# Optimization experiments

Measured on AMD Instinct MI355X. Metric: run time of the kernel, lower is better.

The kernel has to match this reference:

```python
import jax, jax.numpy as jnp
import numpy as np

B, T, C = 2, 2048, 1024
H = 16
HD = C // H  # head_dim = 64
SCALE = HD ** -0.5

def setup_inputs() -> dict:
    key = jax.random.key(0)
    ks = jax.random.split(key, 5)
    s = 1.0 / np.sqrt(C)
    return {
        "x": jax.random.normal(ks[0], (B, T, C), dtype=jnp.float32),
        "Wq": jax.random.normal(ks[1], (C, C), dtype=jnp.float32) * s,
        "Wk": jax.random.normal(ks[2], (C, C), dtype=jnp.float32) * s,
        "Wv": jax.random.normal(ks[3], (C, C), dtype=jnp.float32) * s,
        "Wp": jax.random.normal(ks[4], (C, C), dtype=jnp.float32) * s,
        "bp": jnp.zeros((C,), dtype=jnp.float32),
    }

def reference(x, Wq, Wk, Wv, Wp, bp):
    b, t, c = x.shape
    # QKV projections (no bias, qkv_bias=False) -> [B,T,H,HD]
    q = (x @ Wq).reshape(b, t, H, HD)
    k = (x @ Wk).reshape(b, t, H, HD)
    v = (x @ Wv).reshape(b, t, H, HD)
    # scores [B,H,T,T]
    scores = jnp.einsum("bqhd,bkhd->bhqk", q, k) * SCALE
    causal = jnp.tril(jnp.ones((t, t), dtype=bool))
    scores = jnp.where(causal, scores, -jnp.inf)
    attn = jax.nn.softmax(scores, axis=-1)  # dropout = identity (eval mode)
    out = jnp.einsum("bhqk,bkhd->bqhd", attn, v).reshape(b, t, c)
    return out @ Wp + bp
```

## Files before the change

### kernel.cpp

```cpp
#include <hip/hip_runtime.h>


typedef __attribute__((ext_vector_type(8))) short shortx8;
typedef __attribute__((ext_vector_type(4))) short shortx4;
typedef __attribute__((ext_vector_type(8))) unsigned short ushortx8;
typedef __attribute__((ext_vector_type(4))) float f32x4;
typedef __attribute__((ext_vector_type(16))) float f32x16;

#define MFMA16(a, b, c) __builtin_amdgcn_mfma_f32_16x16x32_bf16((a), (b), (c), 0, 0, 0)
#define MFMA32(a, b, c) __builtin_amdgcn_mfma_f32_32x32x16_bf16((a), (b), (c), 0, 0, 0)

#define SC_L2E 0.18033688011112042f

__device__ __forceinline__ unsigned short f2bf(float f) {
  union { float f; unsigned u; } v; v.f = f;
  unsigned r = v.u + 0x7fffu + ((v.u >> 16) & 1u);
  return (unsigned short)(r >> 16);
}

__device__ __forceinline__ unsigned cvtpk(float a, float b) {
  unsigned r;
  asm("v_cvt_pk_bf16_f32 %0, %1, %2" : "=v"(r) : "v"(a), "v"(b));
  return r;
}

__device__ __forceinline__ float fexp2(float x) {
#if __has_builtin(__builtin_amdgcn_exp2f)
  return __builtin_amdgcn_exp2f(x);
#else
  return exp2f(x);
#endif
}

__device__ __forceinline__ void gload16(const void* g, void* l) {
  __builtin_amdgcn_global_load_lds(
      (const __attribute__((address_space(1))) void*)g,
      (__attribute__((address_space(3))) void*)l, 16, 0, 0);
}

__global__ __launch_bounds__(256) void cvt_x(const float* __restrict__ x,
                                             unsigned short* __restrict__ xb, int n4) {
  int i = blockIdx.x * 256 + threadIdx.x;
  if (i < n4) {
    float4 v = ((const float4*)x)[i];
    unsigned short* o = xb + (size_t)i * 4;
    o[0] = f2bf(v.x); o[1] = f2bf(v.y); o[2] = f2bf(v.z); o[3] = f2bf(v.w);
  }
}

__global__ __launch_bounds__(256) void transpose_w4(
    const float* __restrict__ Wq, const float* __restrict__ Wk,
    const float* __restrict__ Wv, const float* __restrict__ Wp,
    unsigned short* __restrict__ wqkvT, unsigned short* __restrict__ wpT) {
  __shared__ float tile[32][33];
  const int zi = blockIdx.z;
  const float* src = (zi == 0) ? Wq : (zi == 1) ? Wk : (zi == 2) ? Wv : Wp;
  unsigned short* dst = (zi == 3) ? wpT : wqkvT + (size_t)zi * 1048576;
  const int bx = blockIdx.x * 32, by = blockIdx.y * 32;
  const int tx = threadIdx.x & 31, ty = threadIdx.x >> 5;
  #pragma unroll
  for (int i = 0; i < 32; i += 8)
    tile[ty + i][tx] = src[(size_t)(by + ty + i) * 1024 + bx + tx];
  __syncthreads();
  #pragma unroll
  for (int i = 0; i < 32; i += 8)
    dst[(size_t)(bx + ty + i) * 1024 + by + tx] = f2bf(tile[tx][ty + i]);
}

__global__ __launch_bounds__(256) void gemm_bt(
    const unsigned short* __restrict__ A, const unsigned short* __restrict__ BT,
    unsigned short* __restrict__ Cb, float* __restrict__ Cf,
    const float* __restrict__ bias, int M, int N, int K,
    float qscale, int scale_cols, unsigned short* __restrict__ vTo) {
  __shared__ unsigned short As[2][128 * 32];
  __shared__ unsigned short Bs[2][128 * 32];
  const int tid = threadIdx.x;
  const int lane = tid & 63, w = tid >> 6;
  const int wr = w >> 1, wc = w & 1;
  const int brow = blockIdx.y << 7, bcol = blockIdx.x << 7;

  f32x4 z = {0.f, 0.f, 0.f, 0.f};
  f32x4 acc[4][4];
  #pragma unroll
  for (int m = 0; m < 4; ++m)
    #pragma unroll
    for (int n = 0; n < 4; ++n) acc[m][n] = z;

  const int srow = tid >> 2;
  const int scol = (tid & 3) << 3;
  const unsigned short* Ap = A + (size_t)(brow + srow) * K + scol;
  const unsigned short* Bp = BT + (size_t)(bcol + srow) * K + scol;
  const size_t rowK64 = (size_t)64 * K;

  #define GSTAGE(k0_, bi_)                                   \
    do {                                                     \
      unsigned short* AsW = &As[bi_][w * 512];               \
      unsigned short* BsW = &Bs[bi_][w * 512];               \
      gload16(Ap + (k0_), AsW);                              \
      gload16(Ap + rowK64 + (k0_), AsW + 2048);              \
      gload16(Bp + (k0_), BsW);                              \
      gload16(Bp + rowK64 + (k0_), BsW + 2048);              \
    } while (0)

  const int koff = (lane >> 4) << 3;
  const int ar = (wr << 6) + (lane & 15);
  const int br = (wc << 6) + (lane & 15);
  const int nt = K >> 5;
  int bufi = 0;
  GSTAGE(0, 0);
  for (int t = 0; t < nt; ++t) {
    if (t + 1 < nt) {
      GSTAGE((size_t)(t + 1) << 5, bufi ^ 1);
      asm volatile("s_waitcnt vmcnt(4)" ::: "memory");
    } else {
      asm volatile("s_waitcnt vmcnt(0)" ::: "memory");
    }
    __builtin_amdgcn_sched_barrier(0);
    __builtin_amdgcn_s_barrier();
    __builtin_amdgcn_sched_barrier(0);
    shortx8 af[4], bf[4];
    #pragma unroll
    for (int m = 0; m < 4; ++m) af[m] = *(const shortx8*)&As[bufi][(ar + m * 16) * 32 + koff];
    #pragma unroll
    for (int n = 0; n < 4; ++n) bf[n] = *(const shortx8*)&Bs[bufi][(br + n * 16) * 32 + koff];
    #pragma unroll
    for (int m = 0; m < 4; ++m)
      #pragma unroll
      for (int n = 0; n < 4; ++n) acc[m][n] = MFMA16(af[m], bf[n], acc[m][n]);
    asm volatile("s_waitcnt lgkmcnt(0)" ::: "memory");
    __builtin_amdgcn_sched_barrier(0);
    __builtin_amdgcn_s_barrier();
    __builtin_amdgcn_sched_barrier(0);
    bufi ^= 1;
  }
  #undef GSTAGE

  const int r0 = (lane >> 4) << 2;
  const int c0 = lane & 15;
  if (Cb) {
    if (vTo && bcol >= 2048) {
      #pragma unroll
      for (int m = 0; m < 4; ++m)
        #pragma unroll
        for (int n = 0; n < 4; ++n) {
          const int dp = bcol - 2048 + (wc << 6) + n * 16 + c0;
          const size_t rowb = brow + (wr << 6) + m * 16 + r0;
          uint2 u;
          u.x = cvtpk(acc[m][n][0], acc[m][n][1]);
          u.y = cvtpk(acc[m][n][2], acc[m][n][3]);
          *(uint2*)&vTo[(size_t)dp * 4096 + rowb] = u;
        }
    } else {
      #pragma unroll
      for (int m = 0; m < 4; ++m)
        #pragma unroll
        for (int n = 0; n < 4; ++n)
          #pragma unroll
          for (int j = 0; j < 4; ++j) {
            const size_t row = brow + (wr << 6) + m * 16 + r0 + j;
            const size_t col = bcol + (wc << 6) + n * 16 + c0;
            float v = acc[m][n][j];
            if ((int)col < scale_cols) v *= qscale;
            Cb[row * N + col] = f2bf(v);
          }
    }
  } else {
    #pragma unroll
    for (int m = 0; m < 4; ++m)
      #pragma unroll
      for (int n = 0; n < 4; ++n)
        #pragma unroll
        for (int j = 0; j < 4; ++j) {
          const size_t row = brow + (wr << 6) + m * 16 + r0 + j;
          const size_t col = bcol + (wc << 6) + n * 16 + c0;
          Cf[row * N + col] = acc[m][n][j] + bias[col];
        }
  }
}


__global__ __launch_bounds__(256, 4) void attn_fwd(
    const unsigned short* __restrict__ qkv, const unsigned short* __restrict__ vT,
    unsigned short* __restrict__ att) {
  __shared__ unsigned short sh[4][4096];

  const int tid = threadIdx.x;
  const int lane = tid & 63;
  const int p = tid >> 6;
  const int stream = blockIdx.x;
  const int h = stream & 15, b = stream >> 4;
  const int qb = 63 - (int)blockIdx.y;
  const int ql = lane & 31;
  const int hi = lane >> 5;
  const int q = qb * 32 + ql;

  shortx8 qf[4];
  {
    const unsigned short* qp = qkv + ((size_t)(b * 2048 + q)) * 3072 + h * 64 + 8 * hi;
    #pragma unroll
    for (int kc = 0; kc < 4; ++kc) qf[kc] = *(const shortx8*)(qp + 16 * kc);
  }

  f32x16 z16;
  #pragma unroll
  for (int i = 0; i < 16; ++i) z16[i] = 0.f;
  f32x16 accO0 = z16, accO1 = z16;
  float m_run = -__builtin_inff(), l_run = 0.f;

  const unsigned short* kb[4];
  const unsigned short* vb[4];
  #pragma unroll
  for (int i = 0; i < 4; ++i) {
    const int krow = 8 * i + (lane >> 3);
    const int kcl = (lane & 7) ^ (((krow >> 1) ^ (krow >> 4)) & 7);
    kb[i] = qkv + ((size_t)(b * 2048 + krow)) * 3072 + 1024 + h * 64 + 8 * kcl;
    const int vrow = 16 * i + (lane >> 2);
    const int vcl = (lane & 3) ^ (((vrow >> 1) ^ (vrow >> 3)) & 3);
    vb[i] = vT + ((size_t)(h * 64 + vrow)) * 4096 + b * 2048 + 8 * vcl;
  }
  const int rs8 = ((ql >> 1) ^ (ql >> 4)) & 7;
  const int rs4 = ((ql >> 1) ^ (ql >> 3)) & 3;

  unsigned short* Kl = &sh[p][0];
  unsigned short* Vl = &sh[p][2048];

  #define STAGE(t_)                                                        \
    do {                                                                   \
      _Pragma("unroll")                                                    \
      for (int i = 0; i < 4; ++i) {                                        \
        gload16(kb[i] + (size_t)(t_) * 32 * 3072, Kl + i * 512);           \
        gload16(vb[i] + (t_) * 32, Vl + i * 512);                          \
      }                                                                    \
    } while (0)

  if (p <= qb) STAGE(p);
  for (int t = p; t <= qb; t += 4) {
    asm volatile("s_waitcnt vmcnt(0)" ::: "memory");
    __builtin_amdgcn_sched_barrier(0);

    shortx8 kf[4];
    #pragma unroll
    for (int kc = 0; kc < 4; ++kc)
      kf[kc] = *(const shortx8*)&Kl[ql * 64 + 8 * ((2 * kc + hi) ^ rs8)];
    shortx8 vf[2][2];
    #pragma unroll
    for (int dh = 0; dh < 2; ++dh)
      #pragma unroll
      for (int ks = 0; ks < 2; ++ks)
        vf[dh][ks] = *(const shortx8*)&Vl[(32 * dh + ql) * 32 + 8 * ((2 * ks + hi) ^ rs4)];
    asm volatile("s_waitcnt lgkmcnt(0)" ::: "memory");
    __builtin_amdgcn_sched_barrier(0);

    if (t + 4 <= qb) STAGE(t + 4);

    __builtin_amdgcn_s_setprio(1);
    f32x16 s = z16;
    #pragma unroll
    for (int kc = 0; kc < 4; ++kc) s = MFMA32(kf[kc], qf[kc], s);
    __builtin_amdgcn_s_setprio(0);

    if (t == qb) {
      #pragma unroll
      for (int r = 0; r < 16; ++r) {
        const int kvl = (r & 3) + 8 * (r >> 2) + 4 * hi;
        if (kvl > ql) s[r] = -__builtin_inff();
      }
    }

    float m8[8], m4[4];
    #pragma unroll
    for (int i = 0; i < 8; ++i) m8[i] = fmaxf(s[2 * i], s[2 * i + 1]);
    #pragma unroll
    for (int i = 0; i < 4; ++i) m4[i] = fmaxf(m8[2 * i], m8[2 * i + 1]);
    float mx = fmaxf(fmaxf(m4[0], m4[1]), fmaxf(m4[2], m4[3]));
    mx = fmaxf(mx, __shfl_xor(mx, 32));

    if (!__all(mx <= m_run + 8.0f)) {
      const float nm = fmaxf(m_run, mx);
      const float alpha = fexp2(m_run - nm);
      l_run *= alpha;
      #pragma unroll
      for (int r = 0; r < 16; ++r) { accO0[r] *= alpha; accO1[r] *= alpha; }
      m_run = nm;
    }

    #pragma unroll
    for (int r = 0; r < 16; ++r) s[r] = fexp2(s[r] - m_run);
    float a8[8], a4[4];
    #pragma unroll
    for (int i = 0; i < 8; ++i) a8[i] = s[2 * i] + s[2 * i + 1];
    #pragma unroll
    for (int i = 0; i < 4; ++i) a4[i] = a8[2 * i] + a8[2 * i + 1];
    float rsum = (a4[0] + a4[1]) + (a4[2] + a4[3]);
    rsum += __shfl_xor(rsum, 32);
    l_run += rsum;

    unsigned wv[8], xv[8];
    #pragma unroll
    for (int i = 0; i < 8; ++i) wv[i] = cvtpk(s[2 * i], s[2 * i + 1]);
    #pragma unroll
    for (int i = 0; i < 8; ++i) xv[i] = __shfl_xor(wv[i], 32);
    __builtin_amdgcn_s_setprio(1);
    #pragma unroll
    for (int ss = 0; ss < 2; ++ss) {
      union { unsigned u[4]; shortx8 s8; } pb;
      pb.u[0] = hi ? xv[4 * ss + 2] : wv[4 * ss];
      pb.u[1] = hi ? xv[4 * ss + 3] : wv[4 * ss + 1];
      pb.u[2] = hi ? wv[4 * ss + 2] : xv[4 * ss];
      pb.u[3] = hi ? wv[4 * ss + 3] : xv[4 * ss + 1];
      accO0 = MFMA32(vf[0][ss], pb.s8, accO0);
      accO1 = MFMA32(vf[1][ss], pb.s8, accO1);
    }
    __builtin_amdgcn_s_setprio(0);
  }
  #undef STAGE

  float* fb = (float*)&sh[0][0];
  #define DUMP(slot_)                                                          \
    do {                                                                       \
      float* ob = fb + (slot_) * 2048;                                         \
      _Pragma("unroll")                                                        \
      for (int rg = 0; rg < 4; ++rg) {                                         \
        f32x4 v0 = {accO0[4 * rg], accO0[4 * rg + 1],                          \
                    accO0[4 * rg + 2], accO0[4 * rg + 3]};                     \
        f32x4 v1 = {accO1[4 * rg], accO1[4 * rg + 1],                          \
                    accO1[4 * rg + 2], accO1[4 * rg + 3]};                     \
        *(f32x4*)&ob[(rg * 64 + lane) * 4] = v0;                               \
        *(f32x4*)&ob[((4 + rg) * 64 + lane) * 4] = v1;                         \
      }                                                                        \
      fb[4096 + (slot_) * 128 + lane] = m_run;                                 \
      fb[4096 + (slot_) * 128 + 64 + lane] = l_run;                            \
    } while (0)
  #define MERGE(slot_)                                                         \
    do {                                                                       \
      const float m2 = fb[4096 + (slot_) * 128 + lane];                        \
      const float l2 = fb[4096 + (slot_) * 128 + 64 + lane];                   \
      if (m2 != -__builtin_inff()) {                                           \
        float* ob = fb + (slot_) * 2048;                                       \
        const float mf = fmaxf(m_run, m2);                                     \
        const float a1 = fexp2(m_run - mf);                                    \
        const float a2 = fexp2(m2 - mf);                                       \
        _Pragma("unroll")                                                      \
        for (int rg = 0; rg < 4; ++rg) {                                       \
          f32x4 p0 = *(const f32x4*)&ob[(rg * 64 + lane) * 4];                 \
          f32x4 p1 = *(const f32x4*)&ob[((4 + rg) * 64 + lane) * 4];           \
          _Pragma("unroll")                                                    \
          for (int j = 0; j < 4; ++j) {                                        \
            accO0[4 * rg + j] = accO0[4 * rg + j] * a1 + p0[j] * a2;           \
            accO1[4 * rg + j] = accO1[4 * rg + j] * a1 + p1[j] * a2;           \
          }                                                                    \
        }                                                                      \
        l_run = l_run * a1 + l2 * a2;                                          \
        m_run = mf;                                                            \
      }                                                                        \
    } while (0)

  __syncthreads();
  if (p == 1) DUMP(0);
  if (p == 3) DUMP(1);
  __syncthreads();
  if (p == 0) MERGE(0);
  if (p == 2) MERGE(1);
  __syncthreads();
  if (p == 2) DUMP(0);
  __syncthreads();
  if (p == 0) {
    MERGE(0);
    const float inv = 1.f / l_run;
    unsigned short* op = att + ((size_t)(b * 2048 + q)) * 1024 + h * 64;
    #pragma unroll
    for (int rq = 0; rq < 4; ++rq) {
      shortx4 o0, o1;
      #pragma unroll
      for (int j = 0; j < 4; ++j) {
        o0[j] = (short)f2bf(accO0[4 * rq + j] * inv);
        o1[j] = (short)f2bf(accO1[4 * rq + j] * inv);
      }
      *(shortx4*)&op[8 * rq + 4 * hi] = o0;
      *(shortx4*)&op[32 + 8 * rq + 4 * hi] = o1;
    }
  }
  #undef DUMP
  #undef MERGE
}

extern "C" void kernel_launch(void* const* d_in, const int* in_sizes, int n_in,
                              void* d_out, int out_size, void* d_ws, size_t ws_size,
                              hipStream_t stream) {
  const float* x  = (const float*)d_in[0];
  const float* Wq = (const float*)d_in[1];
  const float* Wk = (const float*)d_in[2];
  const float* Wv = (const float*)d_in[3];
  const float* Wp = (const float*)d_in[4];
  const float* bp = (const float*)d_in[5];

  char* ws = (char*)d_ws;
  unsigned short* xb    = (unsigned short*)(ws);
  unsigned short* wqkvT = (unsigned short*)(ws + (size_t)8  * 1048576);
  unsigned short* wpT   = (unsigned short*)(ws + (size_t)14 * 1048576);
  unsigned short* qkv   = (unsigned short*)(ws + (size_t)16 * 1048576);
  unsigned short* vT    = (unsigned short*)(ws + (size_t)40 * 1048576);
  unsigned short* att   = (unsigned short*)(ws + (size_t)48 * 1048576);

  cvt_x<<<dim3(4096), dim3(256), 0, stream>>>(x, xb, 1048576);
  transpose_w4<<<dim3(32, 32, 4), dim3(256), 0, stream>>>(Wq, Wk, Wv, Wp, wqkvT, wpT);
  gemm_bt<<<dim3(24, 32), dim3(256), 0, stream>>>(xb, wqkvT, qkv, nullptr, nullptr,
                                                  4096, 3072, 1024, SC_L2E, 1024, vT);
  attn_fwd<<<dim3(32, 64), dim3(256), 0, stream>>>(qkv, vT, att);
  gemm_bt<<<dim3(8, 32), dim3(256), 0, stream>>>(att, wpT, nullptr, (float*)d_out, bp,
                                                 4096, 1024, 1024, 0.f, 0, nullptr);
}
```

Before: 114.3 us.

## Triple-buffer GEMM loads and use permlane32 swap for attention lane exchange

The projection GEMM moves from a double-buffered to a triple-buffered LDS pipeline, prefetching two K tiles ahead with adjusted vmcnt waits to hide more global load latency. In the attention kernel, cross-half-wave exchanges that used __shfl_xor (ds_bpermute through LDS hardware) are replaced with v_permlane32_swap, which swaps register halves directly and removes the select logic. LDS use per GEMM block grows by half, which may reduce occupancy.

```diff
diff --git a/kernel.cpp b/kernel.cpp
--- a/kernel.cpp
+++ b/kernel.cpp
@@ -6,6 +6,7 @@
 typedef __attribute__((ext_vector_type(8))) unsigned short ushortx8;
 typedef __attribute__((ext_vector_type(4))) float f32x4;
 typedef __attribute__((ext_vector_type(16))) float f32x16;
+typedef __attribute__((ext_vector_type(2))) unsigned uintx2;
 
 #define MFMA16(a, b, c) __builtin_amdgcn_mfma_f32_16x16x32_bf16((a), (b), (c), 0, 0, 0)
 #define MFMA32(a, b, c) __builtin_amdgcn_mfma_f32_32x32x16_bf16((a), (b), (c), 0, 0, 0)
@@ -30,6 +31,21 @@
 #else
   return exp2f(x);
 #endif
+}
+
+__device__ __forceinline__ uintx2 plswap(unsigned a, unsigned b) {
+#if __has_builtin(__builtin_amdgcn_permlane32_swap)
+  return __builtin_amdgcn_permlane32_swap(a, b, false, false);
+#else
+  asm volatile("v_permlane32_swap_b32 %0, %1" : "+v"(a), "+v"(b));
+  uintx2 r; r[0] = a; r[1] = b; return r;
+#endif
+}
+
+__device__ __forceinline__ float partner32(float x, int hi) {
+  unsigned u = __builtin_bit_cast(unsigned, x);
+  uintx2 r = plswap(u, u);
+  return __builtin_bit_cast(float, hi ? r[0] : r[1]);
 }
 
 __device__ __forceinline__ void gload16(const void* g, void* l) {
@@ -72,8 +88,8 @@
     unsigned short* __restrict__ Cb, float* __restrict__ Cf,
     const float* __restrict__ bias, int M, int N, int K,
     float qscale, int scale_cols, unsigned short* __restrict__ vTo) {
-  __shared__ unsigned short As[2][128 * 32];
-  __shared__ unsigned short Bs[2][128 * 32];
+  __shared__ unsigned short As[3][4096];
+  __shared__ unsigned short Bs[3][4096];
   const int tid = threadIdx.x;
   const int lane = tid & 63, w = tid >> 6;
   const int wr = w >> 1, wc = w & 1;
@@ -106,11 +122,15 @@
   const int ar = (wr << 6) + (lane & 15);
   const int br = (wc << 6) + (lane & 15);
   const int nt = K >> 5;
-  int bufi = 0;
+  int cur = 0, sb = 2;
   GSTAGE(0, 0);
+  GSTAGE(32, 1);
   for (int t = 0; t < nt; ++t) {
-    if (t + 1 < nt) {
-      GSTAGE((size_t)(t + 1) << 5, bufi ^ 1);
+    if (t + 2 < nt) {
+      GSTAGE((size_t)(t + 2) << 5, sb);
+      sb = (sb == 2) ? 0 : sb + 1;
+      asm volatile("s_waitcnt vmcnt(8)" ::: "memory");
+    } else if (t + 1 < nt) {
       asm volatile("s_waitcnt vmcnt(4)" ::: "memory");
     } else {
       asm volatile("s_waitcnt vmcnt(0)" ::: "memory");
@@ -120,9 +140,9 @@
     __builtin_amdgcn_sched_barrier(0);
     shortx8 af[4], bf[4];
     #pragma unroll
-    for (int m = 0; m < 4; ++m) af[m] = *(const shortx8*)&As[bufi][(ar + m * 16) * 32 + koff];
-    #pragma unroll
-    for (int n = 0; n < 4; ++n) bf[n] = *(const shortx8*)&Bs[bufi][(br + n * 16) * 32 + koff];
+    for (int m = 0; m < 4; ++m) af[m] = *(const shortx8*)&As[cur][(ar + m * 16) * 32 + koff];
+    #pragma unroll
+    for (int n = 0; n < 4; ++n) bf[n] = *(const shortx8*)&Bs[cur][(br + n * 16) * 32 + koff];
     #pragma unroll
     for (int m = 0; m < 4; ++m)
       #pragma unroll
@@ -131,7 +151,7 @@
     __builtin_amdgcn_sched_barrier(0);
     __builtin_amdgcn_s_barrier();
     __builtin_amdgcn_sched_barrier(0);
-    bufi ^= 1;
+    cur = (cur == 2) ? 0 : cur + 1;
   }
   #undef GSTAGE
 
@@ -273,7 +293,7 @@
     #pragma unroll
     for (int i = 0; i < 4; ++i) m4[i] = fmaxf(m8[2 * i], m8[2 * i + 1]);
     float mx = fmaxf(fmaxf(m4[0], m4[1]), fmaxf(m4[2], m4[3]));
-    mx = fmaxf(mx, __shfl_xor(mx, 32));
+    mx = fmaxf(mx, partner32(mx, hi));
 
     if (!__all(mx <= m_run + 8.0f)) {
       const float nm = fmaxf(m_run, mx);
@@ -292,22 +312,22 @@
     #pragma unroll
     for (int i = 0; i < 4; ++i) a4[i] = a8[2 * i] + a8[2 * i + 1];
     float rsum = (a4[0] + a4[1]) + (a4[2] + a4[3]);
-    rsum += __shfl_xor(rsum, 32);
+    rsum += partner32(rsum, hi);
     l_run += rsum;
 
-    unsigned wv[8], xv[8];
+    unsigned wv[8];
     #pragma unroll
     for (int i = 0; i < 8; ++i) wv[i] = cvtpk(s[2 * i], s[2 * i + 1]);
-    #pragma unroll
-    for (int i = 0; i < 8; ++i) xv[i] = __shfl_xor(wv[i], 32);
     __builtin_amdgcn_s_setprio(1);
     #pragma unroll
     for (int ss = 0; ss < 2; ++ss) {
+      uintx2 r02 = plswap(wv[4 * ss], wv[4 * ss + 2]);
+      uintx2 r13 = plswap(wv[4 * ss + 1], wv[4 * ss + 3]);
       union { unsigned u[4]; shortx8 s8; } pb;
-      pb.u[0] = hi ? xv[4 * ss + 2] : wv[4 * ss];
-      pb.u[1] = hi ? xv[4 * ss + 3] : wv[4 * ss + 1];
-      pb.u[2] = hi ? wv[4 * ss + 2] : xv[4 * ss];
-      pb.u[3] = hi ? wv[4 * ss + 3] : xv[4 * ss + 1];
+      pb.u[0] = r02[0];
+      pb.u[1] = r13[0];
+      pb.u[2] = r02[1];
+      pb.u[3] = r13[1];
       accO0 = MFMA32(vf[0][ss], pb.s8, accO0);
       accO1 = MFMA32(vf[1][ss], pb.s8, accO1);
     }
```

New measurement: 111.5 us. -2.4%, faster.
